# Performance work log

Measured on AMD Instinct MI355X. Metric: run time of the kernel, lower is better.

The kernel has to match this reference:

```python
import jax, jax.numpy as jnp
import numpy as np

B, S, H = 4, 2048, 1024
NH, HD = 16, 64
P = 64            # num persistent vectors
INTER = 2048      # memory MLP intermediate size
LR, MOM, WD = 0.01, 0.9, 0.01
EPS = 1e-12


def setup_inputs() -> dict:
    key = jax.random.key(0)
    ks = jax.random.split(key, 12)
    inp = {
        'hidden_states': jax.random.normal(ks[0], (B, S, H), jnp.float32),
        'k_mem': jax.random.normal(ks[1], (B, S, H), jnp.float32),
        'v_mem': jax.random.normal(ks[2], (B, S, H), jnp.float32),
        # persistent-memory params
        'persistent_vectors': jax.random.normal(ks[3], (P, H), jnp.float32) * 0.02,
        'Wq': jax.random.normal(ks[4], (H, H), jnp.float32) * 0.02,
        'bq': jnp.zeros((H,), jnp.float32),
        'Wo': jax.random.normal(ks[5], (H, H), jnp.float32) * 0.02,
        'bo': jnp.zeros((H,), jnp.float32),
        'ln_g': jnp.ones((H,), jnp.float32),
        'ln_b': jnp.zeros((H,), jnp.float32),
        # surprise-memory MLP params (x @ W1 + b1 -> relu -> @ W2 + b2)
        'W1': jax.random.normal(ks[6], (H, INTER), jnp.float32) * 0.02,
        'b1': jnp.zeros((INTER,), jnp.float32),
        'W2': jax.random.normal(ks[7], (INTER, H), jnp.float32) * 0.02,
        'b2': jnp.zeros((H,), jnp.float32),
        # momentum buffers
        'mW1': jnp.zeros((H, INTER), jnp.float32),
        'mb1': jnp.zeros((INTER,), jnp.float32),
        'mW2': jnp.zeros((INTER, H), jnp.float32),
        'mb2': jnp.zeros((H,), jnp.float32),
    }
    return inp


def _layernorm(x, g, b):
    mu = jnp.mean(x, axis=-1, keepdims=True)
    var = jnp.var(x, axis=-1, keepdims=True)
    return (x - mu) * jax.lax.rsqrt(var + EPS) * g + b


def _mlp(x, W1, b1, W2, b2):
    return jax.nn.relu(x @ W1 + b1) @ W2 + b2


def reference(hidden_states, k_mem, v_mem, persistent_vectors, Wq, bq, Wo, bo,
              ln_g, ln_b, W1, b1, W2, b2, mW1, mb1, mW2, mb2):
    # ---- PersistentMemory: cross-attention to persistent vectors ----
    residual = hidden_states
    hs_norm = _layernorm(hidden_states, ln_g, ln_b)
    q = hs_norm @ Wq + bq                                   # [B,S,H]
    q = q.reshape(B, S, NH, HD).transpose(0, 2, 1, 3)        # [B,nh,S,hd]
    kv = persistent_vectors.reshape(P, NH, HD).transpose(1, 0, 2)  # [nh,P,hd]
    scores = jnp.einsum('bhsd,hpd->bhsp', q, kv) / jnp.sqrt(jnp.float32(HD))
    probs = jax.nn.softmax(scores, axis=-1)
    attn = jnp.einsum('bhsp,hpd->bhsd', probs, kv)           # [B,nh,S,hd]
    attn = attn.transpose(0, 2, 1, 3).reshape(B, S, H)
    out1 = residual + (attn @ Wo + bo)

    # ---- SurpriseMemoryMLP: test-time SGD-with-momentum update (no outer grad) ----
    k_flat = jax.lax.stop_gradient(k_mem.reshape(-1, H))
    v_flat = jax.lax.stop_gradient(v_mem.reshape(-1, H))

    def assoc_loss(params):
        w1, bb1, w2, bb2 = params
        pred = _mlp(k_flat, w1, bb1, w2, bb2)
        return jnp.mean((pred - v_flat) ** 2)

    params = (jax.lax.stop_gradient(W1), jax.lax.stop_gradient(b1),
              jax.lax.stop_gradient(W2), jax.lax.stop_gradient(b2))
    loss, grads = jax.value_and_grad(assoc_loss)(params)

    def upd(p, m, g):
        new_m = MOM * m - LR * g
        return (1.0 - WD) * p + new_m, new_m
    nW1, _ = upd(params[0], mW1, grads[0])
    nb1, _ = upd(params[1], mb1, grads[1])
    nW2, _ = upd(params[2], mW2, grads[2])
    nb2, _ = upd(params[3], mb2, grads[3])

    # ---- query updated memory (torch.no_grad -> stop_gradient) ----
    mem_out = _mlp(out1.reshape(-1, H), nW1, nb1, nW2, nb2).reshape(B, S, H)
    mem_out = jax.lax.stop_gradient(mem_out)

    return out1 + mem_out
```

## Files before the change

### kernel.cpp

```cpp
#include <hip/hip_runtime.h>
#include <hip/hip_bf16.h>

constexpr int B  = 4;
constexpr int S  = 2048;
constexpr int H  = 1024;
constexpr int NH = 16;
constexpr int HD = 64;
constexpr int P  = 64;
constexpr int INTER = 2048;
constexpr int M  = B * S;

typedef __bf16  bf16x8   __attribute__((ext_vector_type(8)));
typedef float   floatx4  __attribute__((ext_vector_type(4)));
typedef float   floatx16 __attribute__((ext_vector_type(16)));

#define AS1 __attribute__((address_space(1)))
#define AS3 __attribute__((address_space(3)))
#define VMCNT(n) asm volatile("s_waitcnt vmcnt(" #n ")" ::: "memory")

__global__ __launch_bounds__(256) void mc_ln_kernel(
    const float* __restrict__ x, const float* __restrict__ g,
    const float* __restrict__ b, __bf16* __restrict__ y)
{
    int row = blockIdx.x;
    const float4* xr = (const float4*)(x + (size_t)row * H);
    float4 v = xr[threadIdx.x];
    float s  = v.x + v.y + v.z + v.w;
    float s2 = v.x*v.x + v.y*v.y + v.z*v.z + v.w*v.w;
    #pragma unroll
    for (int off = 32; off > 0; off >>= 1) {
        s  += __shfl_down(s,  off);
        s2 += __shfl_down(s2, off);
    }
    __shared__ float ws1[4], ws2[4];
    __shared__ float smu, srv;
    int lane = threadIdx.x & 63, wid = threadIdx.x >> 6;
    if (lane == 0) { ws1[wid] = s; ws2[wid] = s2; }
    __syncthreads();
    if (threadIdx.x == 0) {
        float t1 = ws1[0] + ws1[1] + ws1[2] + ws1[3];
        float t2 = ws2[0] + ws2[1] + ws2[2] + ws2[3];
        float mu  = t1 * (1.0f / H);
        float var = t2 * (1.0f / H) - mu * mu;
        smu = mu;
        srv = rsqrtf(var + 1e-12f);
    }
    __syncthreads();
    float mu = smu, rv = srv;
    float4 gv = ((const float4*)g)[threadIdx.x];
    float4 bv = ((const float4*)b)[threadIdx.x];
    union { ushort4 u; __bf16 h[4]; } pk;
    pk.h[0] = (__bf16)((v.x - mu) * rv * gv.x + bv.x);
    pk.h[1] = (__bf16)((v.y - mu) * rv * gv.y + bv.y);
    pk.h[2] = (__bf16)((v.z - mu) * rv * gv.z + bv.z);
    pk.h[3] = (__bf16)((v.w - mu) * rv * gv.w + bv.w);
    ((ushort4*)(y + (size_t)row * H))[threadIdx.x] = pk.u;
}

__global__ __launch_bounds__(256) void mc_trans_kernel(
    const float* __restrict__ src0, const float* __restrict__ mom0,
    __bf16* __restrict__ dst0,
    const float* __restrict__ src1, const float* __restrict__ mom1,
    __bf16* __restrict__ dst1,
    int Rdim, int Cdim, int do_upd)
{
    const float* src = blockIdx.z ? src1 : src0;
    const float* mom = blockIdx.z ? mom1 : mom0;
    __bf16*      dst = blockIdx.z ? dst1 : dst0;
    __shared__ float ts[32][33];
    int c0 = blockIdx.x * 32, r0 = blockIdx.y * 32;
    int tx = threadIdx.x & 31, ty0 = threadIdx.x >> 5;
    #pragma unroll
    for (int i = 0; i < 4; i++) {
        int r = ty0 + i * 8;
        size_t idx = (size_t)(r0 + r) * Cdim + c0 + tx;
        float v = src[idx];
        if (do_upd) v = 0.99f * v + 0.9f * mom[idx];
        ts[r][tx] = v;
    }
    __syncthreads();
    #pragma unroll
    for (int i = 0; i < 4; i++) {
        int r = ty0 + i * 8;
        dst[(size_t)(c0 + r) * Rdim + r0 + tx] = (__bf16)ts[tx][r];
    }
}

__global__ void mc_upd_kernel(const float* __restrict__ b1, const float* __restrict__ mb1,
                              float* __restrict__ nb1,
                              const float* __restrict__ b2, const float* __restrict__ mb2,
                              float* __restrict__ nb2)
{
    int i = blockIdx.x * blockDim.x + threadIdx.x;
    if (i < INTER) nb1[i] = 0.99f * b1[i] + 0.9f * mb1[i];
    else {
        int j = i - INTER;
        if (j < H) nb2[j] = 0.99f * b2[j] + 0.9f * mb2[j];
    }
}

template<int BN, int WMW>
__global__ __launch_bounds__(512, 2) void mc_gemm_p(
    const __bf16* __restrict__ A, const __bf16* __restrict__ Bt,
    const float* __restrict__ bias,
    const float* __restrict__ resF, const __bf16* __restrict__ resB,
    float* __restrict__ outF, __bf16* __restrict__ outB,
    int Ndim, int Kdim, int do_relu)
{
    static_assert(BN == 128 || BN == 256, "BN");
    constexpr int WNW = 8 / WMW;
    constexpr int WR  = 256 / WMW;
    constexpr int WC  = BN / WNW;
    constexpr int FM  = WR / 16;
    constexpr int FN  = WC / 16;
    constexpr int ASLOT = 256 * 32;
    constexpr int BSLOT = BN * 32;
    __shared__ __bf16 lds[4 * ASLOT + 4 * BSLOT];

    int tid  = threadIdx.x;
    int lane = tid & 63;
    int w    = tid >> 6;
    int wm   = w / WNW;
    int wn   = w % WNW;
    int l16  = lane & 15;
    int quad = lane >> 4;

    int gid  = blockIdx.x;
    int wgid = (gid & 7) * 32 + (gid >> 3);
    int by   = wgid >> 3, bx = wgid & 7;
    int m0   = by * 256,  n0 = bx * BN;

    const int NT = Kdim >> 5;

    int f0 = tid, f1 = 512 + tid;
    int r0s = f0 >> 2, c0s = (f0 & 3) ^ ((r0s >> 1) & 3);
    int r1s = f1 >> 2, c1s = (f1 & 3) ^ ((r1s >> 1) & 3);
    const __bf16* aS0 = A  + (size_t)(m0 + r0s) * Kdim + c0s * 8;
    const __bf16* aS1 = A  + (size_t)(m0 + r1s) * Kdim + c1s * 8;
    const __bf16* bS0 = Bt + (size_t)(n0 + r0s) * Kdim + c0s * 8;
    const __bf16* bS1 = Bt + (size_t)(n0 + r1s) * Kdim + c1s * 8;

    auto stage = [&](int t, int s) {
        int k0 = t * 32;
        __builtin_amdgcn_global_load_lds((const AS1 void*)(aS0 + k0),
            (AS3 void*)(lds + s * ASLOT + f0 * 8), 16, 0, 0);
        __builtin_amdgcn_global_load_lds((const AS1 void*)(aS1 + k0),
            (AS3 void*)(lds + s * ASLOT + f1 * 8), 16, 0, 0);
        __builtin_amdgcn_global_load_lds((const AS1 void*)(bS0 + k0),
            (AS3 void*)(lds + 4 * ASLOT + s * BSLOT + f0 * 8), 16, 0, 0);
        if constexpr (BN == 256)
            __builtin_amdgcn_global_load_lds((const AS1 void*)(bS1 + k0),
                (AS3 void*)(lds + 4 * ASLOT + s * BSLOT + f1 * 8), 16, 0, 0);
    };

    int aoff[FM], boff[FN];
    #pragma unroll
    for (int i = 0; i < FM; i++) {
        int row = wm * WR + i * 16 + l16;
        aoff[i] = row * 32 + ((quad ^ ((row >> 1) & 3)) * 8);
    }
    #pragma unroll
    for (int j = 0; j < FN; j++) {
        int row = wn * WC + j * 16 + l16;
        boff[j] = row * 32 + ((quad ^ ((row >> 1) & 3)) * 8);
    }

    stage(0, 0); stage(1, 1); stage(2, 2);
    if constexpr (BN == 256) VMCNT(8); else VMCNT(6);
    __builtin_amdgcn_s_barrier();
    __builtin_amdgcn_sched_barrier(0);

    floatx4 acc[FM][FN] = {};

    for (int t = 0; t < NT; t++) {
        int s = t & 3;
        if (t + 3 < NT) stage(t + 3, (t + 3) & 3);

        const __bf16* Ab = lds + s * ASLOT;
        const __bf16* Bb = lds + 4 * ASLOT + s * BSLOT;
        bf16x8 af[FM], bfr[FN];
        #pragma unroll
        for (int i = 0; i < FM; i++)
            af[i] = *(const bf16x8*)&Ab[aoff[i]];
        #pragma unroll
        for (int j = 0; j < FN; j++)
            bfr[j] = *(const bf16x8*)&Bb[boff[j]];
        __builtin_amdgcn_s_setprio(1);
        #pragma unroll
        for (int i = 0; i < FM; i++)
            #pragma unroll
            for (int j = 0; j < FN; j++)
                acc[i][j] = __builtin_amdgcn_mfma_f32_16x16x32_bf16(
                    af[i], bfr[j], acc[i][j], 0, 0, 0);
        __builtin_amdgcn_s_setprio(0);

        if (t + 1 < NT) {
            if (t + 3 < NT)      { if constexpr (BN == 256) VMCNT(8); else VMCNT(6); }
            else if (t + 2 < NT) { if constexpr (BN == 256) VMCNT(4); else VMCNT(3); }
            else                 VMCNT(0);
            __builtin_amdgcn_s_barrier();
            __builtin_amdgcn_sched_barrier(0);
        }
    }

    #pragma unroll
    for (int i = 0; i < FM; i++) {
        #pragma unroll
        for (int j = 0; j < FN; j++) {
            int col = n0 + wn * WC + j * 16 + l16;
            float bv = bias ? bias[col] : 0.0f;
            #pragma unroll
            for (int r = 0; r < 4; r++) {
                int row = m0 + wm * WR + i * 16 + quad * 4 + r;
                size_t idx = (size_t)row * Ndim + col;
                float v = acc[i][j][r] + bv;
                if (resF)    v += resF[idx];
                if (resB)    v += (float)resB[idx];
                if (do_relu) v  = fmaxf(v, 0.0f);
                if (outF) outF[idx] = v;
                if (outB) outB[idx] = (__bf16)v;
            }
        }
    }
}

constexpr int QLD = 136;
constexpr int KLD = 72;

__global__ __launch_bounds__(256) void mc_qattn(
    const __bf16* __restrict__ A,
    const __bf16* __restrict__ Bt,
    const float* __restrict__ bq,
    const float* __restrict__ pv,
    __bf16* __restrict__ attn)
{
    __shared__ __bf16 Qs[128 * QLD];
    __shared__ union {
        struct { __bf16 As[128 * 64]; __bf16 Bs[128 * 64]; } g;
        struct { __bf16 Ks[64 * KLD]; __bf16 KTs[64 * KLD];
                 __bf16 Ps[128 * KLD]; } a;
    } u;

    int tid  = threadIdx.x;
    int lane = tid & 63;
    int w    = tid >> 6;
    int l16  = lane & 15;
    int quad = lane >> 4;
    int sw   = l16 & 7;

    int hp = blockIdx.x;
    int m0 = blockIdx.y * 128;
    int n0 = hp * 128;

    int wm = (w >> 1) * 64, wn = (w & 1) * 64;
    floatx4 acc[4][4] = {};
    for (int k0 = 0; k0 < H; k0 += 64) {
        #pragma unroll
        for (int t = 0; t < 4; t++) {
            int f = t * 256 + tid;
            int r = f >> 3, c = (f & 7) ^ (r & 7);
            __builtin_amdgcn_global_load_lds(
                (const AS1 void*)(A + (size_t)(m0 + r) * H + k0 + c * 8),
                (AS3 void*)(u.g.As + f * 8), 16, 0, 0);
        }
        #pragma unroll
        for (int t = 0; t < 4; t++) {
            int f = t * 256 + tid;
            int r = f >> 3, c = (f & 7) ^ (r & 7);
            __builtin_amdgcn_global_load_lds(
                (const AS1 void*)(Bt + (size_t)(n0 + r) * H + k0 + c * 8),
                (AS3 void*)(u.g.Bs + f * 8), 16, 0, 0);
        }
        __syncthreads();
        #pragma unroll
        for (int ks = 0; ks < 2; ks++) {
            int cq = ((ks << 2) | quad) ^ sw;
            bf16x8 af[4], bfr[4];
            #pragma unroll
            for (int i = 0; i < 4; i++)
                af[i] = *(const bf16x8*)&u.g.As[(wm + i * 16 + l16) * 64 + cq * 8];
            #pragma unroll
            for (int j = 0; j < 4; j++)
                bfr[j] = *(const bf16x8*)&u.g.Bs[(wn + j * 16 + l16) * 64 + cq * 8];
            #pragma unroll
            for (int i = 0; i < 4; i++)
                #pragma unroll
                for (int j = 0; j < 4; j++)
                    acc[i][j] = __builtin_amdgcn_mfma_f32_16x16x32_bf16(
                        af[i], bfr[j], acc[i][j], 0, 0, 0);
        }
        __syncthreads();
    }

    #pragma unroll
    for (int i = 0; i < 4; i++) {
        #pragma unroll
        for (int j = 0; j < 4; j++) {
            int col = wn + j * 16 + l16;
            float bv = bq[n0 + col];
            #pragma unroll
            for (int r = 0; r < 4; r++) {
                int row = wm + i * 16 + quad * 4 + r;
                Qs[row * QLD + col] = (__bf16)(acc[i][j][r] + bv);
            }
        }
    }

    int rbase = w * 32;
    #pragma unroll
    for (int hh = 0; hh < 2; hh++) {
        int gh = 2 * hp + hh;
        __syncthreads();
        for (int i = tid; i < 64 * 64; i += 256) {
            int p = i >> 6, d = i & 63;
            __bf16 bv = (__bf16)pv[(size_t)p * H + gh * 64 + d];
            u.a.Ks[p * KLD + d]  = bv;
            u.a.KTs[d * KLD + p] = bv;
        }
        __syncthreads();

        floatx4 sc[2][4] = {};
        #pragma unroll
        for (int ks = 0; ks < 2; ks++) {
            bf16x8 aq[2], bk[4];
            #pragma unroll
            for (int i = 0; i < 2; i++)
                aq[i] = *(const bf16x8*)&Qs[(rbase + i * 16 + l16) * QLD +
                                            hh * 64 + ks * 32 + quad * 8];
            #pragma unroll
            for (int j = 0; j < 4; j++)
                bk[j] = *(const bf16x8*)&u.a.Ks[(j * 16 + l16) * KLD + ks * 32 + quad * 8];
            #pragma unroll
            for (int i = 0; i < 2; i++)
                #pragma unroll
                for (int j = 0; j < 4; j++)
                    sc[i][j] = __builtin_amdgcn_mfma_f32_16x16x32_bf16(
                        aq[i], bk[j], sc[i][j], 0, 0, 0);
        }

        #pragma unroll
        for (int i = 0; i < 2; i++) {
            #pragma unroll
            for (int r = 0; r < 4; r++) {
                float v0 = sc[i][0][r] * 0.125f;
                float v1 = sc[i][1][r] * 0.125f;
                float v2 = sc[i][2][r] * 0.125f;
                float v3 = sc[i][3][r] * 0.125f;
                float mx = fmaxf(fmaxf(v0, v1), fmaxf(v2, v3));
                #pragma unroll
                for (int off = 8; off > 0; off >>= 1) mx = fmaxf(mx, __shfl_xor(mx, off));
                float e0 = __expf(v0 - mx), e1 = __expf(v1 - mx);
                float e2 = __expf(v2 - mx), e3 = __expf(v3 - mx);
                float sm = e0 + e1 + e2 + e3;
                #pragma unroll
                for (int off = 8; off > 0; off >>= 1) sm += __shfl_xor(sm, off);
                float inv = __frcp_rn(sm);
                int row = rbase + i * 16 + quad * 4 + r;
                u.a.Ps[row * KLD +  0 + l16] = (__bf16)(e0 * inv);
                u.a.Ps[row * KLD + 16 + l16] = (__bf16)(e1 * inv);
                u.a.Ps[row * KLD + 32 + l16] = (__bf16)(e2 * inv);
                u.a.Ps[row * KLD + 48 + l16] = (__bf16)(e3 * inv);
            }
        }
        __syncthreads();

        floatx4 ov[2][4] = {};
        #pragma unroll
        for (int ks = 0; ks < 2; ks++) {
            bf16x8 ap[2], bkt[4];
            #pragma unroll
            for (int i = 0; i < 2; i++)
                ap[i] = *(const bf16x8*)&u.a.Ps[(rbase + i * 16 + l16) * KLD + ks * 32 + quad * 8];
            #pragma unroll
            for (int j = 0; j < 4; j++)
                bkt[j] = *(const bf16x8*)&u.a.KTs[(j * 16 + l16) * KLD + ks * 32 + quad * 8];
            #pragma unroll
            for (int i = 0; i < 2; i++)
                #pragma unroll
                for (int j = 0; j < 4; j++)
                    ov[i][j] = __builtin_amdgcn_mfma_f32_16x16x32_bf16(
                        ap[i], bkt[j], ov[i][j], 0, 0, 0);
        }

        #pragma unroll
        for (int i = 0; i < 2; i++) {
            #pragma unroll
            for (int j = 0; j < 4; j++) {
                int col = j * 16 + l16;
                #pragma unroll
                for (int r = 0; r < 4; r++) {
                    int row = rbase + i * 16 + quad * 4 + r;
                    attn[(size_t)(m0 + row) * H + gh * 64 + col] = (__bf16)ov[i][j][r];
                }
            }
        }
    }
}

extern "C" void kernel_launch(void* const* d_in, const int* in_sizes, int n_in,
                              void* d_out, int out_size, void* d_ws, size_t ws_size,
                              hipStream_t stream)
{
    const float* hidden = (const float*)d_in[0];
    const float* pv   = (const float*)d_in[3];
    const float* Wq   = (const float*)d_in[4];
    const float* bq   = (const float*)d_in[5];
    const float* Wo   = (const float*)d_in[6];
    const float* bo   = (const float*)d_in[7];
    const float* ln_g = (const float*)d_in[8];
    const float* ln_b = (const float*)d_in[9];
    const float* W1   = (const float*)d_in[10];
    const float* b1   = (const float*)d_in[11];
    const float* W2   = (const float*)d_in[12];
    const float* b2   = (const float*)d_in[13];
    const float* mW1  = (const float*)d_in[14];
    const float* mb1  = (const float*)d_in[15];
    const float* mW2  = (const float*)d_in[16];
    const float* mb2  = (const float*)d_in[17];

    float* out = (float*)d_out;
    char*  wsb = (char*)d_ws;

    constexpr size_t MB = 1024 * 1024;
    __bf16* normb  = (__bf16*)(wsb);
    __bf16* attnb  = (__bf16*)(wsb + 16  * MB);
    __bf16* out1b  = (__bf16*)(wsb + 32  * MB);
    __bf16* hb     = (__bf16*)(wsb + 48  * MB);
    __bf16* Wqt    = (__bf16*)(wsb + 80  * MB);
    __bf16* Wot    = (__bf16*)(wsb + 82  * MB);
    __bf16* W1t    = (__bf16*)(wsb + 84  * MB);
    __bf16* W2t    = (__bf16*)(wsb + 88  * MB);
    float*  nb1    = (float*) (wsb + 92  * MB);
    float*  nb2    = (float*) (wsb + 92  * MB + 8192);

    mc_trans_kernel<<<dim3(32, 32, 2), 256, 0, stream>>>(
        Wq, nullptr, Wqt, Wo, nullptr, Wot, H, H, 0);
    mc_trans_kernel<<<dim3(64, 32, 1), 256, 0, stream>>>(
        W1, mW1, W1t, nullptr, nullptr, nullptr, H, INTER, 1);
    mc_trans_kernel<<<dim3(32, 64, 1), 256, 0, stream>>>(
        W2, mW2, W2t, nullptr, nullptr, nullptr, INTER, H, 1);
    mc_upd_kernel<<<(INTER + H + 255) / 256, 256, 0, stream>>>(b1, mb1, nb1, b2, mb2, nb2);

    mc_ln_kernel<<<M, 256, 0, stream>>>(hidden, ln_g, ln_b, normb);

    mc_qattn<<<dim3(NH / 2, M / 128), 256, 0, stream>>>(normb, Wqt, bq, pv, attnb);

    mc_gemm_p<128, 4><<<256, 512, 0, stream>>>(attnb, Wot, bo, hidden, nullptr,
                                               nullptr, out1b, H, H, 0);

    mc_gemm_p<256, 2><<<256, 512, 0, stream>>>(out1b, W1t, nb1, nullptr, nullptr,
                                               nullptr, hb, INTER, H, 1);

    mc_gemm_p<128, 4><<<256, 512, 0, stream>>>(hb, W2t, nb2, nullptr, out1b,
                                               out, nullptr, H, INTER, 0);
}
```

Before: 358.1 us.

## Restructure GEMM mainloop into 64-wide K tiles with quadrant-split ping-pong staging

The GEMM main loop moves from a 4-stage ring of 32-wide K slices to a double-buffered scheme with 64-wide K tiles. Each tile's compute is split into four output quadrants, and global-to-LDS loads for the next tile are issued in halves between quadrant MFMA batches. The LDS swizzle changes to an 8-way XOR on the 64-wide row. The aim is fewer barriers per K step, better overlap of copies with MFMAs, and fewer repeated LDS fragment reloads, at the cost of a shallower prefetch depth and more intricate vmcnt bookkeeping.

```diff
diff --git a/kernel.cpp b/kernel.cpp
--- a/kernel.cpp
+++ b/kernel.cpp
@@ -12,7 +12,6 @@
 
 typedef __bf16  bf16x8   __attribute__((ext_vector_type(8)));
 typedef float   floatx4  __attribute__((ext_vector_type(4)));
-typedef float   floatx16 __attribute__((ext_vector_type(16)));
 
 #define AS1 __attribute__((address_space(1)))
 #define AS3 __attribute__((address_space(3)))
@@ -107,15 +106,15 @@
     float* __restrict__ outF, __bf16* __restrict__ outB,
     int Ndim, int Kdim, int do_relu)
 {
-    static_assert(BN == 128 || BN == 256, "BN");
     constexpr int WNW = 8 / WMW;
     constexpr int WR  = 256 / WMW;
     constexpr int WC  = BN / WNW;
-    constexpr int FM  = WR / 16;
-    constexpr int FN  = WC / 16;
-    constexpr int ASLOT = 256 * 32;
-    constexpr int BSLOT = BN * 32;
-    __shared__ __bf16 lds[4 * ASLOT + 4 * BSLOT];
+    constexpr int FM  = WR / 16, FN = WC / 16;
+    constexpr int FMH = FM / 2,  FNH = FN / 2;
+    constexpr int ABUF = 256 * 64;
+    constexpr int BBUF = BN * 64;
+    constexpr int BI   = BN / 128;
+    __shared__ alignas(128) __bf16 lds[2 * ABUF + 2 * BBUF];
 
     int tid  = threadIdx.x;
     int lane = tid & 63;
@@ -130,77 +129,165 @@
     int by   = wgid >> 3, bx = wgid & 7;
     int m0   = by * 256,  n0 = bx * BN;
 
-    const int NT = Kdim >> 5;
-
-    int f0 = tid, f1 = 512 + tid;
-    int r0s = f0 >> 2, c0s = (f0 & 3) ^ ((r0s >> 1) & 3);
-    int r1s = f1 >> 2, c1s = (f1 & 3) ^ ((r1s >> 1) & 3);
-    const __bf16* aS0 = A  + (size_t)(m0 + r0s) * Kdim + c0s * 8;
-    const __bf16* aS1 = A  + (size_t)(m0 + r1s) * Kdim + c1s * 8;
-    const __bf16* bS0 = Bt + (size_t)(n0 + r0s) * Kdim + c0s * 8;
-    const __bf16* bS1 = Bt + (size_t)(n0 + r1s) * Kdim + c1s * 8;
-
-    auto stage = [&](int t, int s) {
-        int k0 = t * 32;
-        __builtin_amdgcn_global_load_lds((const AS1 void*)(aS0 + k0),
-            (AS3 void*)(lds + s * ASLOT + f0 * 8), 16, 0, 0);
-        __builtin_amdgcn_global_load_lds((const AS1 void*)(aS1 + k0),
-            (AS3 void*)(lds + s * ASLOT + f1 * 8), 16, 0, 0);
-        __builtin_amdgcn_global_load_lds((const AS1 void*)(bS0 + k0),
-            (AS3 void*)(lds + 4 * ASLOT + s * BSLOT + f0 * 8), 16, 0, 0);
-        if constexpr (BN == 256)
-            __builtin_amdgcn_global_load_lds((const AS1 void*)(bS1 + k0),
-                (AS3 void*)(lds + 4 * ASLOT + s * BSLOT + f1 * 8), 16, 0, 0);
+    const int NT = Kdim >> 6;
+
+    const __bf16* aSrc[2][2]; int aDst[2][2];
+    const __bf16* bSrc[2][2]; int bDst[2][2];
+    #pragma unroll
+    for (int h = 0; h < 2; h++) {
+        #pragma unroll
+        for (int p = 0; p < 2; p++) {
+            int g = (p * 8 + w) * 8 + (lane >> 3);
+            constexpr int HS = WR / 2;
+            int r = (g / HS) * WR + h * HS + (g % HS);
+            int cg = (lane & 7) ^ (r & 7);
+            aSrc[h][p] = A + (size_t)(m0 + r) * Kdim + cg * 8;
+            aDst[h][p] = r * 64 + (lane & 7) * 8;
+        }
+        #pragma unroll
+        for (int p = 0; p < BI; p++) {
+            int g = (p * 8 + w) * 8 + (lane >> 3);
+            constexpr int HS = WC / 2;
+            int r = (g / HS) * WC + h * HS + (g % HS);
+            int cg = (lane & 7) ^ (r & 7);
+            bSrc[h][p] = Bt + (size_t)(n0 + r) * Kdim + cg * 8;
+            bDst[h][p] = r * 64 + (lane & 7) * 8;
+        }
+    }
+
+    auto stageA = [&](int kt, int h) {
+        int k0 = kt * 64;
+        __bf16* dst = lds + (kt & 1) * ABUF;
+        #pragma unroll
+        for (int p = 0; p < 2; p++)
+            __builtin_amdgcn_global_load_lds((const AS1 void*)(aSrc[h][p] + k0),
+                (AS3 void*)(dst + aDst[h][p]), 16, 0, 0);
     };
-
-    int aoff[FM], boff[FN];
+    auto stageB = [&](int kt, int h) {
+        int k0 = kt * 64;
+        __bf16* dst = lds + 2 * ABUF + (kt & 1) * BBUF;
+        #pragma unroll
+        for (int p = 0; p < BI; p++)
+            __builtin_amdgcn_global_load_lds((const AS1 void*)(bSrc[h][p] + k0),
+                (AS3 void*)(dst + bDst[h][p]), 16, 0, 0);
+    };
+
+    int aoff[FM][2], boff[FN][2];
     #pragma unroll
     for (int i = 0; i < FM; i++) {
         int row = wm * WR + i * 16 + l16;
-        aoff[i] = row * 32 + ((quad ^ ((row >> 1) & 3)) * 8);
+        #pragma unroll
+        for (int kk = 0; kk < 2; kk++)
+            aoff[i][kk] = row * 64 + ((((kk << 2) | quad) ^ (row & 7)) * 8);
     }
     #pragma unroll
     for (int j = 0; j < FN; j++) {
         int row = wn * WC + j * 16 + l16;
-        boff[j] = row * 32 + ((quad ^ ((row >> 1) & 3)) * 8);
-    }
-
-    stage(0, 0); stage(1, 1); stage(2, 2);
-    if constexpr (BN == 256) VMCNT(8); else VMCNT(6);
+        #pragma unroll
+        for (int kk = 0; kk < 2; kk++)
+            boff[j][kk] = row * 64 + ((((kk << 2) | quad) ^ (row & 7)) * 8);
+    }
+
+    stageA(0, 0); stageB(0, 0); stageB(0, 1); stageA(0, 1);
+    VMCNT(0);
     __builtin_amdgcn_s_barrier();
     __builtin_amdgcn_sched_barrier(0);
 
     floatx4 acc[FM][FN] = {};
 
-    for (int t = 0; t < NT; t++) {
-        int s = t & 3;
-        if (t + 3 < NT) stage(t + 3, (t + 3) & 3);
-
-        const __bf16* Ab = lds + s * ASLOT;
-        const __bf16* Bb = lds + 4 * ASLOT + s * BSLOT;
-        bf16x8 af[FM], bfr[FN];
-        #pragma unroll
-        for (int i = 0; i < FM; i++)
-            af[i] = *(const bf16x8*)&Ab[aoff[i]];
-        #pragma unroll
-        for (int j = 0; j < FN; j++)
-            bfr[j] = *(const bf16x8*)&Bb[boff[j]];
-        __builtin_amdgcn_s_setprio(1);
-        #pragma unroll
-        for (int i = 0; i < FM; i++)
-            #pragma unroll
-            for (int j = 0; j < FN; j++)
-                acc[i][j] = __builtin_amdgcn_mfma_f32_16x16x32_bf16(
-                    af[i], bfr[j], acc[i][j], 0, 0, 0);
-        __builtin_amdgcn_s_setprio(0);
-
-        if (t + 1 < NT) {
-            if (t + 3 < NT)      { if constexpr (BN == 256) VMCNT(8); else VMCNT(6); }
-            else if (t + 2 < NT) { if constexpr (BN == 256) VMCNT(4); else VMCNT(3); }
-            else                 VMCNT(0);
+    for (int kt = 0; kt < NT; kt++) {
+        const __bf16* Ab = lds + (kt & 1) * ABUF;
+        const __bf16* Bb = lds + 2 * ABUF + (kt & 1) * BBUF;
+        bool pre = (kt + 1 < NT);
+
+        bf16x8 ar[FMH][2], br[FNH][2];
+
+        if (kt) {
+            if constexpr (BN == 256) VMCNT(4); else VMCNT(3);
             __builtin_amdgcn_s_barrier();
             __builtin_amdgcn_sched_barrier(0);
         }
+
+        if (pre) stageA(kt + 1, 0);
+        #pragma unroll
+        for (int i = 0; i < FMH; i++) {
+            ar[i][0] = *(const bf16x8*)&Ab[aoff[i][0]];
+            ar[i][1] = *(const bf16x8*)&Ab[aoff[i][1]];
+        }
+        #pragma unroll
+        for (int j = 0; j < FNH; j++) {
+            br[j][0] = *(const bf16x8*)&Bb[boff[j][0]];
+            br[j][1] = *(const bf16x8*)&Bb[boff[j][1]];
+        }
+        __builtin_amdgcn_s_setprio(1);
+        #pragma unroll
+        for (int i = 0; i < FMH; i++)
+            #pragma unroll
+            for (int j = 0; j < FNH; j++)
+                #pragma unroll
+                for (int kk = 0; kk < 2; kk++)
+                    acc[i][j] = __builtin_amdgcn_mfma_f32_16x16x32_bf16(
+                        ar[i][kk], br[j][kk], acc[i][j], 0, 0, 0);
+        __builtin_amdgcn_s_setprio(0);
+        __builtin_amdgcn_sched_barrier(0);
+
+        VMCNT(2);
+        __builtin_amdgcn_s_barrier();
+        __builtin_amdgcn_sched_barrier(0);
+
+        if (pre) stageB(kt + 1, 0);
+        #pragma unroll
+        for (int j = 0; j < FNH; j++) {
+            br[j][0] = *(const bf16x8*)&Bb[boff[FNH + j][0]];
+            br[j][1] = *(const bf16x8*)&Bb[boff[FNH + j][1]];
+        }
+        __builtin_amdgcn_s_setprio(1);
+        #pragma unroll
+        for (int i = 0; i < FMH; i++)
+            #pragma unroll
+            for (int j = 0; j < FNH; j++)
+                #pragma unroll
+                for (int kk = 0; kk < 2; kk++)
+                    acc[i][FNH + j] = __builtin_amdgcn_mfma_f32_16x16x32_bf16(
+                        ar[i][kk], br[j][kk], acc[i][FNH + j], 0, 0, 0);
+        __builtin_amdgcn_s_setprio(0);
+        __builtin_amdgcn_sched_barrier(0);
+
+        if (pre) stageB(kt + 1, 1);
+        #pragma unroll
+        for (int i = 0; i < FMH; i++) {
+            ar[i][0] = *(const bf16x8*)&Ab[aoff[FMH + i][0]];
+            ar[i][1] = *(const bf16x8*)&Ab[aoff[FMH + i][1]];
+        }
+        __builtin_amdgcn_s_setprio(1);
+        #pragma unroll
+        for (int i = 0; i < FMH; i++)
+            #pragma unroll
+            for (int j = 0; j < FNH; j++)
+                #pragma unroll
+                for (int kk = 0; kk < 2; kk++)
+                    acc[FMH + i][FNH + j] = __builtin_amdgcn_mfma_f32_16x16x32_bf16(
+                        ar[i][kk], br[j][kk], acc[FMH + i][FNH + j], 0, 0, 0);
+        __builtin_amdgcn_s_setprio(0);
+        __builtin_amdgcn_sched_barrier(0);
+
+        if (pre) stageA(kt + 1, 1);
+        #pragma unroll
+        for (int j = 0; j < FNH; j++) {
+            br[j][0] = *(const bf16x8*)&Bb[boff[j][0]];
+            br[j][1] = *(const bf16x8*)&Bb[boff[j][1]];
+        }
+        __builtin_amdgcn_s_setprio(1);
+        #pragma unroll
+        for (int i = 0; i < FMH; i++)
+            #pragma unroll
+            for (int j = 0; j < FNH; j++)
+                #pragma unroll
+                for (int kk = 0; kk < 2; kk++)
+                    acc[FMH + i][j] = __builtin_amdgcn_mfma_f32_16x16x32_bf16(
+                        ar[i][kk], br[j][kk], acc[FMH + i][j], 0, 0, 0);
+        __builtin_amdgcn_s_setprio(0);
+        __builtin_amdgcn_sched_barrier(0);
     }
 
     #pragma unroll
```

Result: no change. 354.1 us (-1.1%).

## Split GEMM k-step into two half phases interleaving prefetch with MFMA

Applied to the files above, without the earlier changes.

Restructures the GEMM main loop so each k-step is split into two halves of the M fragments. The A-tile prefetch is issued before the first half of the MFMAs and the B-tile prefetch before the second half, with sched barriers between them. The wait-and-barrier moves to the top of the loop. The aim is to interleave global-to-LDS loads with matrix work and to cut A-fragment register pressure, at the cost of an extra scheduling fence and a finer issue order.

```diff
diff --git a/kernel.cpp b/kernel.cpp
--- a/kernel.cpp
+++ b/kernel.cpp
@@ -12,7 +12,6 @@
 
 typedef __bf16  bf16x8   __attribute__((ext_vector_type(8)));
 typedef float   floatx4  __attribute__((ext_vector_type(4)));
-typedef float   floatx16 __attribute__((ext_vector_type(16)));
 
 #define AS1 __attribute__((address_space(1)))
 #define AS3 __attribute__((address_space(3)))
@@ -107,15 +106,14 @@
     float* __restrict__ outF, __bf16* __restrict__ outB,
     int Ndim, int Kdim, int do_relu)
 {
-    static_assert(BN == 128 || BN == 256, "BN");
     constexpr int WNW = 8 / WMW;
     constexpr int WR  = 256 / WMW;
     constexpr int WC  = BN / WNW;
-    constexpr int FM  = WR / 16;
-    constexpr int FN  = WC / 16;
+    constexpr int FM  = WR / 16, FN = WC / 16;
+    constexpr int FMH = FM / 2;
     constexpr int ASLOT = 256 * 32;
     constexpr int BSLOT = BN * 32;
-    __shared__ __bf16 lds[4 * ASLOT + 4 * BSLOT];
+    __shared__ alignas(128) __bf16 lds[4 * ASLOT + 4 * BSLOT];
 
     int tid  = threadIdx.x;
     int lane = tid & 63;
@@ -140,12 +138,15 @@
     const __bf16* bS0 = Bt + (size_t)(n0 + r0s) * Kdim + c0s * 8;
     const __bf16* bS1 = Bt + (size_t)(n0 + r1s) * Kdim + c1s * 8;
 
-    auto stage = [&](int t, int s) {
-        int k0 = t * 32;
+    auto stageA = [&](int t) {
+        int k0 = t * 32, s = t & 3;
         __builtin_amdgcn_global_load_lds((const AS1 void*)(aS0 + k0),
             (AS3 void*)(lds + s * ASLOT + f0 * 8), 16, 0, 0);
         __builtin_amdgcn_global_load_lds((const AS1 void*)(aS1 + k0),
             (AS3 void*)(lds + s * ASLOT + f1 * 8), 16, 0, 0);
+    };
+    auto stageB = [&](int t) {
+        int k0 = t * 32, s = t & 3;
         __builtin_amdgcn_global_load_lds((const AS1 void*)(bS0 + k0),
             (AS3 void*)(lds + 4 * ASLOT + s * BSLOT + f0 * 8), 16, 0, 0);
         if constexpr (BN == 256)
@@ -165,7 +166,7 @@
         boff[j] = row * 32 + ((quad ^ ((row >> 1) & 3)) * 8);
     }
 
-    stage(0, 0); stage(1, 1); stage(2, 2);
+    stageA(0); stageB(0); stageA(1); stageB(1); stageA(2); stageB(2);
     if constexpr (BN == 256) VMCNT(8); else VMCNT(6);
     __builtin_amdgcn_s_barrier();
     __builtin_amdgcn_sched_barrier(0);
@@ -173,34 +174,49 @@
     floatx4 acc[FM][FN] = {};
 
     for (int t = 0; t < NT; t++) {
-        int s = t & 3;
-        if (t + 3 < NT) stage(t + 3, (t + 3) & 3);
-
-        const __bf16* Ab = lds + s * ASLOT;
-        const __bf16* Bb = lds + 4 * ASLOT + s * BSLOT;
-        bf16x8 af[FM], bfr[FN];
-        #pragma unroll
-        for (int i = 0; i < FM; i++)
-            af[i] = *(const bf16x8*)&Ab[aoff[i]];
-        #pragma unroll
-        for (int j = 0; j < FN; j++)
-            bfr[j] = *(const bf16x8*)&Bb[boff[j]];
-        __builtin_amdgcn_s_setprio(1);
-        #pragma unroll
-        for (int i = 0; i < FM; i++)
-            #pragma unroll
-            for (int j = 0; j < FN; j++)
-                acc[i][j] = __builtin_amdgcn_mfma_f32_16x16x32_bf16(
-                    af[i], bfr[j], acc[i][j], 0, 0, 0);
-        __builtin_amdgcn_s_setprio(0);
-
-        if (t + 1 < NT) {
-            if (t + 3 < NT)      { if constexpr (BN == 256) VMCNT(8); else VMCNT(6); }
-            else if (t + 2 < NT) { if constexpr (BN == 256) VMCNT(4); else VMCNT(3); }
+        const __bf16* Ab = lds + (t & 3) * ASLOT;
+        const __bf16* Bb = lds + 4 * ASLOT + (t & 3) * BSLOT;
+
+        if (t) {
+            if (t + 2 < NT)      { if constexpr (BN == 256) VMCNT(8); else VMCNT(6); }
+            else if (t + 1 < NT) { if constexpr (BN == 256) VMCNT(4); else VMCNT(3); }
             else                 VMCNT(0);
             __builtin_amdgcn_s_barrier();
             __builtin_amdgcn_sched_barrier(0);
         }
+        bool pre = (t + 3 < NT);
+        bf16x8 ar[FMH], br[FN];
+
+        if (pre) stageA(t + 3);
+        #pragma unroll
+        for (int j = 0; j < FN; j++)
+            br[j] = *(const bf16x8*)&Bb[boff[j]];
+        #pragma unroll
+        for (int i = 0; i < FMH; i++)
+            ar[i] = *(const bf16x8*)&Ab[aoff[i]];
+        __builtin_amdgcn_s_setprio(1);
+        #pragma unroll
+        for (int i = 0; i < FMH; i++)
+            #pragma unroll
+            for (int j = 0; j < FN; j++)
+                acc[i][j] = __builtin_amdgcn_mfma_f32_16x16x32_bf16(
+                    ar[i], br[j], acc[i][j], 0, 0, 0);
+        __builtin_amdgcn_s_setprio(0);
+        __builtin_amdgcn_sched_barrier(0);
+
+        if (pre) stageB(t + 3);
+        #pragma unroll
+        for (int i = 0; i < FMH; i++)
+            ar[i] = *(const bf16x8*)&Ab[aoff[FMH + i]];
+        __builtin_amdgcn_s_setprio(1);
+        #pragma unroll
+        for (int i = 0; i < FMH; i++)
+            #pragma unroll
+            for (int j = 0; j < FN; j++)
+                acc[FMH + i][j] = __builtin_amdgcn_mfma_f32_16x16x32_bf16(
+                    ar[i], br[j], acc[FMH + i][j], 0, 0, 0);
+        __builtin_amdgcn_s_setprio(0);
+        __builtin_amdgcn_sched_barrier(0);
     }
 
     #pragma unroll
```

After: 358.7 us. No clear change (+0.2%).
